# Kernel optimization log

Measured on AMD Instinct MI355X. Metric: run time of the kernel, lower is better.

## Reference

```python
import jax, jax.numpy as jnp
import numpy as np

TAU = 1.0
K_TAU = 1.0
MAX_K = 64


def setup_inputs() -> dict:
    key = jax.random.key(0)
    ks = jax.random.split(key, 6)
    B, S, D, H = 8, 4096, 1024, 2048
    token_embeddings = jax.random.normal(ks[0], (B, S, D), dtype=jnp.float32)
    W1 = jax.random.normal(ks[1], (D, H), dtype=jnp.float32) * (1.0 / np.sqrt(D))
    b1 = jnp.zeros((H,), dtype=jnp.float32)
    W2 = jax.random.normal(ks[2], (H, 1), dtype=jnp.float32) * (1.0 / np.sqrt(H))
    b2 = jnp.zeros((1,), dtype=jnp.float32)
    k_logits = jax.random.normal(ks[3], (MAX_K,), dtype=jnp.float32) * 0.02
    return {"token_embeddings": token_embeddings, "W1": W1, "b1": b1,
            "W2": W2, "b2": b2, "k_logits": k_logits}


def _gumbel(rng, shape):
    u = jax.random.uniform(rng, shape, minval=1e-08, maxval=1.0 - 1e-08)
    return -jnp.log(-jnp.log(u))


def reference(token_embeddings, W1, b1, W2, b2, k_logits):
    B, S, D = token_embeddings.shape
    # scorer: Dense -> relu -> Dense(1), squeeze -> [B, S]
    h = jax.nn.relu(jnp.einsum('bsd,dh->bsh', token_embeddings, W1) + b1)
    importance_logits = (jnp.einsum('bsh,ho->bso', h, W2) + b2)[..., 0]

    rng = jax.random.key(42)  # training rng
    rng1, rng2 = jax.random.split(rng)

    # learnable-k selection (training branch)
    k_gumbel = _gumbel(rng1, k_logits.shape)
    k_soft = jax.nn.softmax((k_logits + k_gumbel) / K_TAU)
    expected_k = jnp.sum(k_soft * jnp.arange(1, MAX_K + 1, dtype=k_soft.dtype))
    k_selected = jnp.argmax(k_soft) + 1  # traced int scalar

    # gumbel-softmax hard top-k over tokens
    perturbed = importance_logits + _gumbel(rng2, importance_logits.shape)
    soft_mask = jax.nn.softmax(perturbed / TAU, axis=-1)  # [B, S]
    # rank of each token (0 = smallest); top-k == rank >= S - k
    rank = jnp.argsort(jnp.argsort(soft_mask, axis=-1), axis=-1)
    hard_mask = (rank >= S - k_selected).astype(soft_mask.dtype)
    selection_mask = jax.lax.stop_gradient(hard_mask - soft_mask) + soft_mask

    filtered_embeddings = token_embeddings * selection_mask[..., None]
    return filtered_embeddings, selection_mask, expected_k
```

## Files before the change

### kernel.cpp

```cpp
#include <hip/hip_runtime.h>
#include <stdint.h>

#define B_BATCH 8
#define S_SEQ   4096
#define D_DIM   1024
#define H_DIM   2048
#define M_TOK   (B_BATCH * S_SEQ)
#define MAXK    64
#define NSPLIT  2

typedef unsigned int u32;
typedef unsigned short u16;
typedef unsigned long long u64;
typedef __attribute__((ext_vector_type(8))) short short8;
typedef __attribute__((ext_vector_type(4))) float f32x4;

#define GLOBAL_AS __attribute__((address_space(1)))
#define LDS_AS    __attribute__((address_space(3)))


#define TF_ROUND(x0, x1, r) { x0 += x1; x1 = ((x1 << r) | (x1 >> (32 - r))); x1 ^= x0; }

__device__ __forceinline__ void tf2x32(u32 k0, u32 k1, u32 x0, u32 x1, u32& o0, u32& o1) {
  u32 k2 = k0 ^ k1 ^ 0x1BD11BDAu;
  x0 += k0; x1 += k1;
  TF_ROUND(x0, x1, 13) TF_ROUND(x0, x1, 15) TF_ROUND(x0, x1, 26) TF_ROUND(x0, x1, 6)
  x0 += k1; x1 += k2 + 1u;
  TF_ROUND(x0, x1, 17) TF_ROUND(x0, x1, 29) TF_ROUND(x0, x1, 16) TF_ROUND(x0, x1, 24)
  x0 += k2; x1 += k0 + 2u;
  TF_ROUND(x0, x1, 13) TF_ROUND(x0, x1, 15) TF_ROUND(x0, x1, 26) TF_ROUND(x0, x1, 6)
  x0 += k0; x1 += k1 + 3u;
  TF_ROUND(x0, x1, 17) TF_ROUND(x0, x1, 29) TF_ROUND(x0, x1, 16) TF_ROUND(x0, x1, 24)
  x0 += k1; x1 += k2 + 4u;
  TF_ROUND(x0, x1, 13) TF_ROUND(x0, x1, 15) TF_ROUND(x0, x1, 26) TF_ROUND(x0, x1, 6)
  x0 += k2; x1 += k0 + 5u;
  o0 = x0; o1 = x1;
}

__device__ __forceinline__ void jax_subkeys(u32& r1a, u32& r1b, u32& r2a, u32& r2b) {
  tf2x32(0u, 42u, 0u, 0u, r1a, r1b);
  tf2x32(0u, 42u, 0u, 1u, r2a, r2b);
}

__device__ __forceinline__ u32 jax_bits32(u32 ka, u32 kb, u32 i) {
  u32 o0, o1;
  tf2x32(ka, kb, 0u, i, o0, o1);
  return o0 ^ o1;
}

__device__ __forceinline__ float jax_uniform_from_bits(u32 bits) {
  float f = __uint_as_float((bits >> 9) | 0x3f800000u) - 1.0f;
  float r = f + 1e-8f;
  return fmaxf(1e-8f, r);
}

__device__ __forceinline__ float gumbel_from_bits(u32 bits) {
  float u = jax_uniform_from_bits(bits);
  return -logf(-logf(u));
}

__device__ __forceinline__ u32 ordf(float v) {
  u32 b = __float_as_uint(v);
  return (b & 0x80000000u) ? ~b : (b | 0x80000000u);
}

__device__ __forceinline__ u64 shflx64(u64 v, int m) {
  unsigned lo = (unsigned)v, hi = (unsigned)(v >> 32);
  lo = (unsigned)__shfl_xor((int)lo, m);
  hi = (unsigned)__shfl_xor((int)hi, m);
  return ((u64)hi << 32) | lo;
}


__device__ __forceinline__ u16 f2bf_rn(float x) {
  u32 u = __float_as_uint(x);
  u32 r = u + 0x7fffu + ((u >> 16) & 1u);
  return (u16)(r >> 16);
}

__device__ __forceinline__ void split1(float x, u16& h, u16& lo) {
  h = f2bf_rn(x);
  float hf = __uint_as_float(((u32)h) << 16);
  lo = f2bf_rn(x - hf);
}


__global__ __launch_bounds__(256) void split_a_kernel(const float* __restrict__ x,
                                                      u16* __restrict__ hi,
                                                      u16* __restrict__ lo) {
  const size_t i = ((size_t)blockIdx.x * 256 + threadIdx.x) * 4;
  float4 v = *(const float4*)(x + i);
  u16 h0, h1, h2, h3, l0, l1, l2, l3;
  split1(v.x, h0, l0); split1(v.y, h1, l1); split1(v.z, h2, l2); split1(v.w, h3, l3);
  u64 hv = (u64)h0 | ((u64)h1 << 16) | ((u64)h2 << 32) | ((u64)h3 << 48);
  u64 lv = (u64)l0 | ((u64)l1 << 16) | ((u64)l2 << 32) | ((u64)l3 << 48);
  *(u64*)(hi + i) = hv;
  *(u64*)(lo + i) = lv;
}

__global__ __launch_bounds__(256) void split_w1t_kernel(const float* __restrict__ W1,
                                                        u16* __restrict__ bhi,
                                                        u16* __restrict__ blo) {
  __shared__ float tile[32][33];
  const int tx = threadIdx.x & 31, ty = threadIdx.x >> 5;
  const int n0 = blockIdx.x * 32, k0 = blockIdx.y * 32;
  #pragma unroll
  for (int r = 0; r < 4; ++r)
    tile[ty + r * 8][tx] = W1[(size_t)(k0 + ty + r * 8) * H_DIM + n0 + tx];
  __syncthreads();
  #pragma unroll
  for (int r = 0; r < 4; ++r) {
    const int n = n0 + ty + r * 8, k = k0 + tx;
    u16 h, l;
    split1(tile[tx][ty + r * 8], h, l);
    bhi[(size_t)n * D_DIM + k] = h;
    blo[(size_t)n * D_DIM + k] = l;
  }
}


__device__ __forceinline__ void stage16(const u16* g, u16* l) {
  __builtin_amdgcn_global_load_lds((const GLOBAL_AS u32*)g, (LDS_AS u32*)l, 16, 0, 0);
}

__global__ __launch_bounds__(256, 2) void scorer_mfma(
    const u16* __restrict__ Ahi, const u16* __restrict__ Alo,
    const u16* __restrict__ Bhi, const u16* __restrict__ Blo,
    const float* __restrict__ b1, const float* __restrict__ W2,
    float* __restrict__ pl) {
  __shared__ u16 smem[8 * 128 * 32];
  u16* sAhi = smem;
  u16* sAlo = smem + 8192;
  u16* sBhi = smem + 16384;
  u16* sBlo = smem + 24576;

  const int tid = threadIdx.x;
  const int w = tid >> 6;
  const int l = tid & 63;

  const int b = blockIdx.x;
  const int xcd = b & 7;
  const int nyb = xcd & 1;
  const int m0 = ((b >> 3) * 4 + (xcd >> 1)) * 128;

  const int rl0 = w * 32 + (l >> 2);
  const int rl1 = rl0 + 16;
  const int kloc0 = (((l & 3) ^ ((rl0 >> 1) & 3)) << 3);
  const int kloc1 = (((l & 3) ^ ((rl1 >> 1) & 3)) << 3);
  const int lb0 = (w * 32) * 32;
  const int lb1 = (w * 32 + 16) * 32;

  int a_off[4], b_off[4];
  #pragma unroll
  for (int i = 0; i < 4; ++i) {
    int row = ((w & 1) << 6) + i * 16 + (l & 15);
    int slot = (l >> 4) ^ ((row >> 1) & 3);
    a_off[i] = row * 32 + slot * 8;
    int nrow = ((w >> 1) << 6) + i * 16 + (l & 15);
    int nslot = (l >> 4) ^ ((nrow >> 1) & 3);
    b_off[i] = nrow * 32 + nslot * 8;
  }

  float logit[4][4];
  #pragma unroll
  for (int i = 0; i < 4; ++i)
    #pragma unroll
    for (int r = 0; r < 4; ++r) logit[i][r] = 0.f;

  for (int t8 = 0; t8 < H_DIM / (128 * NSPLIT); ++t8) {
    const int n0 = nyb * (H_DIM / NSPLIT) + t8 * 128;
    f32x4 acc[4][4];
    #pragma unroll
    for (int i = 0; i < 4; ++i)
      #pragma unroll
      for (int j = 0; j < 4; ++j) acc[i][j] = (f32x4){0.f, 0.f, 0.f, 0.f};

    const u16* pA0h = Ahi + (size_t)(m0 + rl0) * D_DIM + kloc0;
    const u16* pA1h = Ahi + (size_t)(m0 + rl1) * D_DIM + kloc1;
    const u16* pA0l = Alo + (size_t)(m0 + rl0) * D_DIM + kloc0;
    const u16* pA1l = Alo + (size_t)(m0 + rl1) * D_DIM + kloc1;
    const u16* pB0h = Bhi + (size_t)(n0 + rl0) * D_DIM + kloc0;
    const u16* pB1h = Bhi + (size_t)(n0 + rl1) * D_DIM + kloc1;
    const u16* pB0l = Blo + (size_t)(n0 + rl0) * D_DIM + kloc0;
    const u16* pB1l = Blo + (size_t)(n0 + rl1) * D_DIM + kloc1;

    for (int k0 = 0; k0 < D_DIM; k0 += 64) {
      __syncthreads();
      #pragma unroll
      for (int s = 0; s < 2; ++s) {
        const int so = s * 4096;
        const int sk = s * 32;
        stage16(pA0h + sk, sAhi + so + lb0); stage16(pA1h + sk, sAhi + so + lb1);
        stage16(pA0l + sk, sAlo + so + lb0); stage16(pA1l + sk, sAlo + so + lb1);
        stage16(pB0h + sk, sBhi + so + lb0); stage16(pB1h + sk, sBhi + so + lb1);
        stage16(pB0l + sk, sBlo + so + lb0); stage16(pB1l + sk, sBlo + so + lb1);
      }
      pA0h += 64; pA1h += 64; pA0l += 64; pA1l += 64;
      pB0h += 64; pB1h += 64; pB0l += 64; pB1l += 64;
      __syncthreads();

      #pragma unroll
      for (int s = 0; s < 2; ++s) {
        const int so = s * 4096;
        short8 ah[4], al[4], bh[4], bl[4];
        #pragma unroll
        for (int i = 0; i < 4; ++i) {
          ah[i] = *(const short8*)(sAhi + so + a_off[i]);
          al[i] = *(const short8*)(sAlo + so + a_off[i]);
          bh[i] = *(const short8*)(sBhi + so + b_off[i]);
          bl[i] = *(const short8*)(sBlo + so + b_off[i]);
        }
        #pragma unroll
        for (int i = 0; i < 4; ++i)
          #pragma unroll
          for (int j = 0; j < 4; ++j) {
            acc[i][j] = __builtin_amdgcn_mfma_f32_16x16x32_bf16(ah[i], bh[j], acc[i][j], 0, 0, 0);
            acc[i][j] = __builtin_amdgcn_mfma_f32_16x16x32_bf16(ah[i], bl[j], acc[i][j], 0, 0, 0);
            acc[i][j] = __builtin_amdgcn_mfma_f32_16x16x32_bf16(al[i], bh[j], acc[i][j], 0, 0, 0);
          }
      }
    }

    const int nb = n0 + ((w >> 1) << 6);
    #pragma unroll
    for (int j = 0; j < 4; ++j) {
      const int n = nb + j * 16 + (l & 15);
      const float b1v = b1[n];
      const float w2v = W2[n];
      #pragma unroll
      for (int i = 0; i < 4; ++i)
        #pragma unroll
        for (int r = 0; r < 4; ++r)
          logit[i][r] += fmaxf(acc[i][j][r] + b1v, 0.f) * w2v;
    }
  }

  __syncthreads();
  float* red = (float*)smem;
  const int col = (l & 15) + ((w >> 1) << 4);
  #pragma unroll
  for (int i = 0; i < 4; ++i)
    #pragma unroll
    for (int r = 0; r < 4; ++r) {
      const int m = ((w & 1) << 6) + i * 16 + ((l >> 4) << 2) + r;
      red[m * 33 + col] = logit[i][r];
    }
  __syncthreads();
  if (tid < 128) {
    float s = 0.f;
    #pragma unroll
    for (int x = 0; x < 32; ++x) s += red[tid * 33 + x];
    pl[(size_t)nyb * M_TOK + m0 + tid] = s;
  }
}


__global__ __launch_bounds__(256) void scorer_kernel(
    const float* __restrict__ emb, const float* __restrict__ W1,
    const float* __restrict__ b1, const float* __restrict__ W2,
    const float* __restrict__ b2, float* __restrict__ pert) {
  __shared__ float As[16][68];
  __shared__ float Bs[16][132];
  __shared__ float red[64][17];

  const int tid = threadIdx.x;
  const int tx = tid & 15;
  const int ty = tid >> 4;
  const int m0 = blockIdx.x * 64;
  const int at = tid >> 2;
  const int ac = (tid & 3) << 2;
  const int br = tid >> 4;
  const int bc = (tid & 15) << 3;

  float logit[4] = {0.f, 0.f, 0.f, 0.f};

  for (int n0 = 0; n0 < H_DIM; n0 += 128) {
    float acc[4][8];
    #pragma unroll
    for (int i = 0; i < 4; i++)
      #pragma unroll
      for (int j = 0; j < 8; j++) acc[i][j] = 0.f;

    for (int k0 = 0; k0 < D_DIM; k0 += 16) {
      float4 av  = *(const float4*)(emb + (size_t)(m0 + at) * D_DIM + (k0 + ac));
      float4 bv0 = *(const float4*)(W1 + (size_t)(k0 + br) * H_DIM + (n0 + bc));
      float4 bv1 = *(const float4*)(W1 + (size_t)(k0 + br) * H_DIM + (n0 + bc) + 4);
      __syncthreads();
      As[ac + 0][at] = av.x; As[ac + 1][at] = av.y;
      As[ac + 2][at] = av.z; As[ac + 3][at] = av.w;
      *(float4*)&Bs[br][bc]     = bv0;
      *(float4*)&Bs[br][bc + 4] = bv1;
      __syncthreads();
      #pragma unroll
      for (int k = 0; k < 16; k++) {
        float4 a   = *(const float4*)&As[k][ty << 2];
        float4 b0  = *(const float4*)&Bs[k][tx << 3];
        float4 b1v = *(const float4*)&Bs[k][(tx << 3) + 4];
        float aa[4] = {a.x, a.y, a.z, a.w};
        float bb[8] = {b0.x, b0.y, b0.z, b0.w, b1v.x, b1v.y, b1v.z, b1v.w};
        #pragma unroll
        for (int i = 0; i < 4; i++)
          #pragma unroll
          for (int j = 0; j < 8; j++)
            acc[i][j] = fmaf(aa[i], bb[j], acc[i][j]);
      }
    }
    float4 c0 = *(const float4*)(b1 + n0 + (tx << 3));
    float4 c1 = *(const float4*)(b1 + n0 + (tx << 3) + 4);
    float4 w0 = *(const float4*)(W2 + n0 + (tx << 3));
    float4 w1 = *(const float4*)(W2 + n0 + (tx << 3) + 4);
    float cb[8] = {c0.x, c0.y, c0.z, c0.w, c1.x, c1.y, c1.z, c1.w};
    float wb[8] = {w0.x, w0.y, w0.z, w0.w, w1.x, w1.y, w1.z, w1.w};
    #pragma unroll
    for (int i = 0; i < 4; i++)
      #pragma unroll
      for (int j = 0; j < 8; j++) {
        float h = fmaxf(acc[i][j] + cb[j], 0.f);
        logit[i] = fmaf(h, wb[j], logit[i]);
      }
  }

  __syncthreads();
  #pragma unroll
  for (int i = 0; i < 4; i++) red[(ty << 2) + i][tx] = logit[i];
  __syncthreads();

  if (tid < 64) {
    float s = 0.f;
    #pragma unroll
    for (int x = 0; x < 16; x++) s += red[tid][x];
    s += b2[0];
    int t = m0 + tid;
    u32 r1a, r1b, r2a, r2b;
    jax_subkeys(r1a, r1b, r2a, r2b);
    pert[t] = s + gumbel_from_bits(jax_bits32(r2a, r2b, (u32)t));
  }
}


template <bool FROM_PL>
__device__ __forceinline__ void topk_body(const float* kl, const float* pl,
                                          const float* b2, float* mask,
                                          float* expk) {
  const int r = blockIdx.x;
  const int tid = threadIdx.x;
  const int w = tid >> 6, l = tid & 63;
  __shared__ int ksel_sh;
  __shared__ int cnt[2][4];

  u32 r1a, r1b, r2a, r2b;
  jax_subkeys(r1a, r1b, r2a, r2b);

  if (tid < 64) {
    float p = kl[l] + gumbel_from_bits(jax_bits32(r1a, r1b, (u32)l));
    u64 kkey = ((u64)ordf(p) << 32) | (unsigned)(63 - l);
    #pragma unroll
    for (int off = 32; off >= 1; off >>= 1) {
      u64 o = shflx64(kkey, off);
      if (o > kkey) kkey = o;
    }
    if (l == 0) ksel_sh = 64 - (int)(kkey & 0xffffffffu);
    if (r == 0) {
      float m = p;
      #pragma unroll
      for (int off = 32; off >= 1; off >>= 1) m = fmaxf(m, __shfl_xor(m, off));
      float e = expf(p - m);
      float s = e;
      #pragma unroll
      for (int off = 32; off >= 1; off >>= 1) s += __shfl_xor(s, off);
      float v = (e / s) * (float)(l + 1);
      #pragma unroll
      for (int off = 32; off >= 1; off >>= 1) v += __shfl_xor(v, off);
      if (l == 0) expk[0] = v;
    }
  }
  __syncthreads();
  const int k = ksel_sh;
  const float b2v = FROM_PL ? b2[0] : 0.f;

  u64 keys[16];
  #pragma unroll
  for (int j = 0; j < 16; j++) {
    int s = tid + (j << 8);
    int t = (r << 12) + s;
    float v;
    if (FROM_PL) {
      float acc = pl[t];
      #pragma unroll
      for (int q = 1; q < NSPLIT; ++q) acc += pl[(size_t)q * M_TOK + t];
      v = acc + b2v + gumbel_from_bits(jax_bits32(r2a, r2b, (u32)t));
    } else {
      v = mask[t];
    }
    keys[j] = ((u64)ordf(v) << 12) | (unsigned)s;
  }

  u64 lo = 0ull, hi = (1ull << 44) - 1ull;
  int it = 0;
  while (lo < hi) {
    const u64 mid = (lo + hi + 1ull) >> 1;
    int c = 0;
    #pragma unroll
    for (int j = 0; j < 16; j++) c += (keys[j] >= mid) ? 1 : 0;
    #pragma unroll
    for (int off = 32; off >= 1; off >>= 1) c += __shfl_xor(c, off);
    const int buf = it & 1;
    if (l == 0) cnt[buf][w] = c;
    __syncthreads();
    const int tot = cnt[buf][0] + cnt[buf][1] + cnt[buf][2] + cnt[buf][3];
    if (tot >= k) lo = mid; else hi = mid - 1ull;
    ++it;
  }
  const u64 thresh = lo;

  #pragma unroll
  for (int j = 0; j < 16; j++) {
    int s = tid + (j << 8);
    mask[(r << 12) + s] = (keys[j] >= thresh) ? 1.0f : 0.0f;
  }
}

__global__ __launch_bounds__(256) void topk_pl_kernel(const float* __restrict__ kl,
                                                      const float* __restrict__ pl,
                                                      const float* __restrict__ b2,
                                                      float* __restrict__ mask,
                                                      float* __restrict__ expk) {
  topk_body<true>(kl, pl, b2, mask, expk);
}

__global__ __launch_bounds__(256) void topk_kernel(const float* __restrict__ kl,
                                                   float* __restrict__ mask,
                                                   float* __restrict__ expk) {
  topk_body<false>(kl, nullptr, nullptr, mask, expk);
}


__global__ __launch_bounds__(256) void filter_kernel(const float* __restrict__ emb,
                                                     const float* __restrict__ mask,
                                                     float* __restrict__ out) {
  const int t = blockIdx.x;
  const float mk = mask[t];
  const size_t base = (size_t)t * D_DIM + ((size_t)threadIdx.x << 2);
  float4 v = *(const float4*)(emb + base);
  *(float4*)(out + base) = make_float4(v.x * mk, v.y * mk, v.z * mk, v.w * mk);
}


extern "C" void kernel_launch(void* const* d_in, const int* in_sizes, int n_in,
                              void* d_out, int out_size, void* d_ws, size_t ws_size,
                              hipStream_t stream) {
  const float* emb = (const float*)d_in[0];
  const float* W1  = (const float*)d_in[1];
  const float* b1  = (const float*)d_in[2];
  const float* W2  = (const float*)d_in[3];
  const float* b2  = (const float*)d_in[4];
  const float* kl  = (const float*)d_in[5];
  float* out  = (float*)d_out;
  float* mask = out + (size_t)M_TOK * D_DIM;
  float* expk = mask + M_TOK;

  const size_t ws_need = (size_t)H_DIM * D_DIM * 2 * 2 + (size_t)NSPLIT * M_TOK * 4;

  if (ws_size >= ws_need) {
    u16* Ahi = (u16*)d_out;
    u16* Alo = Ahi + (size_t)M_TOK * D_DIM;
    u16* Bhi = (u16*)d_ws;
    u16* Blo = Bhi + (size_t)H_DIM * D_DIM;
    float* pl = (float*)(Blo + (size_t)H_DIM * D_DIM);

    split_a_kernel<<<M_TOK * D_DIM / 1024, 256, 0, stream>>>(emb, Ahi, Alo);
    split_w1t_kernel<<<dim3(H_DIM / 32, D_DIM / 32), 256, 0, stream>>>(W1, Bhi, Blo);
    scorer_mfma<<<M_TOK / 128 * NSPLIT, 256, 0, stream>>>(Ahi, Alo, Bhi, Blo, b1, W2, pl);
    topk_pl_kernel<<<B_BATCH, 256, 0, stream>>>(kl, pl, b2, mask, expk);
  } else {
    scorer_kernel<<<M_TOK / 64, 256, 0, stream>>>(emb, W1, b1, W2, b2, mask);
    topk_kernel<<<B_BATCH, 256, 0, stream>>>(kl, mask, expk);
  }

  filter_kernel<<<M_TOK, 256, 0, stream>>>(emb, mask, out);
}
```

Baseline: 702.8 us.

## Rewrite scorer GEMM as 256x256-tile, 512-thread double-buffered pipelined MFMA kernel

Replaces the 128x128-tile scorer GEMM with a 256-row by 256-column tile per block using 8 waves. A/B fragments are staged into a double-buffered dynamic LDS region through async global-to-LDS loads, interleaved with MFMA phases and gated by explicit vmcnt waits and raw barriers. MFMA issue priority is raised while the MFMAs run. The ReLU/W2 epilogue now reduces across lanes with shuffles into an LDS accumulator. The goal is to hide load latency and increase reuse per LDS byte. The cost is 132 KB of LDS per block, a fixed grid of 256 blocks, and hand-tuned wait counts that are fragile.

```diff
diff --git a/kernel.cpp b/kernel.cpp
--- a/kernel.cpp
+++ b/kernel.cpp
@@ -123,134 +123,173 @@
   __builtin_amdgcn_global_load_lds((const GLOBAL_AS u32*)g, (LDS_AS u32*)l, 16, 0, 0);
 }
 
-__global__ __launch_bounds__(256, 2) void scorer_mfma(
+#define WAITV(N) asm volatile("s_waitcnt vmcnt(" #N ")" ::: "memory")
+#define FENCE()  asm volatile("" ::: "memory")
+
+__global__ __launch_bounds__(512, 2) void scorer_mfma256(
     const u16* __restrict__ Ahi, const u16* __restrict__ Alo,
     const u16* __restrict__ Bhi, const u16* __restrict__ Blo,
     const float* __restrict__ b1, const float* __restrict__ W2,
     float* __restrict__ pl) {
-  __shared__ u16 smem[8 * 128 * 32];
-  u16* sAhi = smem;
-  u16* sAlo = smem + 8192;
-  u16* sBhi = smem + 16384;
-  u16* sBlo = smem + 24576;
+  extern __shared__ u16 smem[];
+  float* red = (float*)(smem + 65536);
 
   const int tid = threadIdx.x;
-  const int w = tid >> 6;
-  const int l = tid & 63;
+  const int w = tid >> 6, l = tid & 63;
+  const int wm = w >> 2, wn = w & 3;
 
   const int b = blockIdx.x;
   const int xcd = b & 7;
   const int nyb = xcd & 1;
-  const int m0 = ((b >> 3) * 4 + (xcd >> 1)) * 128;
-
-  const int rl0 = w * 32 + (l >> 2);
-  const int rl1 = rl0 + 16;
-  const int kloc0 = (((l & 3) ^ ((rl0 >> 1) & 3)) << 3);
-  const int kloc1 = (((l & 3) ^ ((rl1 >> 1) & 3)) << 3);
-  const int lb0 = (w * 32) * 32;
-  const int lb1 = (w * 32 + 16) * 32;
-
-  int a_off[4], b_off[4];
-  #pragma unroll
-  for (int i = 0; i < 4; ++i) {
-    int row = ((w & 1) << 6) + i * 16 + (l & 15);
-    int slot = (l >> 4) ^ ((row >> 1) & 3);
-    a_off[i] = row * 32 + slot * 8;
-    int nrow = ((w >> 1) << 6) + i * 16 + (l & 15);
-    int nslot = (l >> 4) ^ ((nrow >> 1) & 3);
-    b_off[i] = nrow * 32 + nslot * 8;
-  }
-
-  float logit[4][4];
-  #pragma unroll
-  for (int i = 0; i < 4; ++i)
-    #pragma unroll
-    for (int r = 0; r < 4; ++r) logit[i][r] = 0.f;
-
-  for (int t8 = 0; t8 < H_DIM / (128 * NSPLIT); ++t8) {
-    const int n0 = nyb * (H_DIM / NSPLIT) + t8 * 128;
-    f32x4 acc[4][4];
-    #pragma unroll
-    for (int i = 0; i < 4; ++i)
-      #pragma unroll
-      for (int j = 0; j < 4; ++j) acc[i][j] = (f32x4){0.f, 0.f, 0.f, 0.f};
-
-    const u16* pA0h = Ahi + (size_t)(m0 + rl0) * D_DIM + kloc0;
-    const u16* pA1h = Ahi + (size_t)(m0 + rl1) * D_DIM + kloc1;
-    const u16* pA0l = Alo + (size_t)(m0 + rl0) * D_DIM + kloc0;
-    const u16* pA1l = Alo + (size_t)(m0 + rl1) * D_DIM + kloc1;
-    const u16* pB0h = Bhi + (size_t)(n0 + rl0) * D_DIM + kloc0;
-    const u16* pB1h = Bhi + (size_t)(n0 + rl1) * D_DIM + kloc1;
-    const u16* pB0l = Blo + (size_t)(n0 + rl0) * D_DIM + kloc0;
-    const u16* pB1l = Blo + (size_t)(n0 + rl1) * D_DIM + kloc1;
-
-    for (int k0 = 0; k0 < D_DIM; k0 += 64) {
-      __syncthreads();
-      #pragma unroll
-      for (int s = 0; s < 2; ++s) {
-        const int so = s * 4096;
-        const int sk = s * 32;
-        stage16(pA0h + sk, sAhi + so + lb0); stage16(pA1h + sk, sAhi + so + lb1);
-        stage16(pA0l + sk, sAlo + so + lb0); stage16(pA1l + sk, sAlo + so + lb1);
-        stage16(pB0h + sk, sBhi + so + lb0); stage16(pB1h + sk, sBhi + so + lb1);
-        stage16(pB0l + sk, sBlo + so + lb0); stage16(pB1l + sk, sBlo + so + lb1);
-      }
-      pA0h += 64; pA1h += 64; pA0l += 64; pA1l += 64;
-      pB0h += 64; pB1h += 64; pB0l += 64; pB1l += 64;
-      __syncthreads();
-
-      #pragma unroll
-      for (int s = 0; s < 2; ++s) {
-        const int so = s * 4096;
-        short8 ah[4], al[4], bh[4], bl[4];
+  const int m0 = ((b >> 3) * 4 + (xcd >> 1)) * 256;
+
+  const int sig = w * 16 + (l >> 2);
+  const int swz = ((l & 3) ^ ((sig >> 1) & 3)) << 3;
+  const size_t aoffE = (size_t)(m0 + sig + (sig & 64)) * D_DIM + swz;
+  const size_t aoffL = aoffE + (size_t)64 * D_DIM;
+  const size_t boff0 = (size_t)(nyb * 1024 + sig) * D_DIM + swz;
+  const size_t boff1 = boff0 + (size_t)128 * D_DIM;
+  u16* const ldsw = smem + w * 512;
+
+#define ST_AhiE(T) stage16(Ahi + aoffE + (size_t)((((T) & 31) << 5)), ldsw + (((T) & 1) << 15) + 0)
+#define ST_AhiL(T) stage16(Ahi + aoffL + (size_t)((((T) & 31) << 5)), ldsw + (((T) & 1) << 15) + 4096)
+#define ST_AloE(T) stage16(Alo + aoffE + (size_t)((((T) & 31) << 5)), ldsw + (((T) & 1) << 15) + 8192)
+#define ST_AloL(T) stage16(Alo + aoffL + (size_t)((((T) & 31) << 5)), ldsw + (((T) & 1) << 15) + 12288)
+#define ST_BhiH0(T) stage16(Bhi + boff0 + ((size_t)((T) >> 5) << 18) + (size_t)((((T) & 31) << 5)), ldsw + (((T) & 1) << 15) + 16384)
+#define ST_BhiH1(T) stage16(Bhi + boff1 + ((size_t)((T) >> 5) << 18) + (size_t)((((T) & 31) << 5)), ldsw + (((T) & 1) << 15) + 20480)
+#define ST_BloH0(T) stage16(Blo + boff0 + ((size_t)((T) >> 5) << 18) + (size_t)((((T) & 31) << 5)), ldsw + (((T) & 1) << 15) + 24576)
+#define ST_BloH1(T) stage16(Blo + boff1 + ((size_t)((T) >> 5) << 18) + (size_t)((((T) & 31) << 5)), ldsw + (((T) & 1) << 15) + 28672)
+
+  int a_off[8], b_off[4];
+  #pragma unroll
+  for (int mf = 0; mf < 8; ++mf) {
+    int slot = wm * 64 + (mf & 3) * 16 + (l & 15);
+    a_off[mf] = ((mf >> 2) * 4096) + slot * 32 + (((l >> 4) ^ ((slot >> 1) & 3)) << 3);
+  }
+  #pragma unroll
+  for (int nf = 0; nf < 4; ++nf) {
+    int r = wn * 64 + nf * 16 + (l & 15);
+    b_off[nf] = r * 32 + (((l >> 4) ^ ((r >> 1) & 3)) << 3);
+  }
+
+  f32x4 acc[8][4];
+  #pragma unroll
+  for (int mf = 0; mf < 8; ++mf)
+    #pragma unroll
+    for (int nf = 0; nf < 4; ++nf) acc[mf][nf] = (f32x4){0.f, 0.f, 0.f, 0.f};
+
+  const u16* const B0 = smem;
+  const u16* const B1 = smem + 32768;
+  short8 ah0, ah1, al0, al1, bh[4], bl[4];
+
+#define LDA(BASE, MF) \
+  ah0 = *(const short8*)((BASE) + a_off[MF]); \
+  ah1 = *(const short8*)((BASE) + a_off[(MF) + 1]); \
+  al0 = *(const short8*)((BASE) + 8192 + a_off[MF]); \
+  al1 = *(const short8*)((BASE) + 8192 + a_off[(MF) + 1])
+
+#define LDB(BASE) \
+  { _Pragma("unroll") \
+    for (int nf = 0; nf < 4; ++nf) { \
+      bh[nf] = *(const short8*)((BASE) + 16384 + b_off[nf]); \
+      bl[nf] = *(const short8*)((BASE) + 24576 + b_off[nf]); \
+    } }
+
+#define MMA2(MF) \
+  __builtin_amdgcn_s_setprio(1); \
+  { _Pragma("unroll") \
+    for (int nf = 0; nf < 4; ++nf) { \
+      acc[MF][nf] = __builtin_amdgcn_mfma_f32_16x16x32_bf16(ah0, bh[nf], acc[MF][nf], 0, 0, 0); \
+      acc[MF][nf] = __builtin_amdgcn_mfma_f32_16x16x32_bf16(ah0, bl[nf], acc[MF][nf], 0, 0, 0); \
+      acc[MF][nf] = __builtin_amdgcn_mfma_f32_16x16x32_bf16(al0, bh[nf], acc[MF][nf], 0, 0, 0); \
+      acc[(MF) + 1][nf] = __builtin_amdgcn_mfma_f32_16x16x32_bf16(ah1, bh[nf], acc[(MF) + 1][nf], 0, 0, 0); \
+      acc[(MF) + 1][nf] = __builtin_amdgcn_mfma_f32_16x16x32_bf16(ah1, bl[nf], acc[(MF) + 1][nf], 0, 0, 0); \
+      acc[(MF) + 1][nf] = __builtin_amdgcn_mfma_f32_16x16x32_bf16(al1, bh[nf], acc[(MF) + 1][nf], 0, 0, 0); \
+    } } \
+  __builtin_amdgcn_s_setprio(0)
+
+  ST_BhiH0(0); ST_BhiH1(0); ST_BloH0(0); ST_BloH1(0);
+  ST_AhiE(0);  ST_AloE(0);  ST_AhiL(0);  ST_AloL(0);
+  ST_BhiH0(1); ST_BhiH1(1); ST_BloH0(1); ST_BloH1(1);
+  ST_AhiE(1);  ST_AloE(1);
+  WAITV(8);
+  __builtin_amdgcn_s_barrier();
+  FENCE();
+
+  for (int it = 0; it < 64; ++it) {
+    const bool last = (it == 63);
+    const int T1 = 2 * it + 1, T2 = 2 * it + 2, T3 = 2 * it + 3;
+
+    LDB(B0); LDA(B0, 0);
+    ST_AhiL(T1); ST_AloL(T1);
+    MMA2(0);
+    __builtin_amdgcn_s_barrier(); FENCE();
+    LDA(B0, 2);
+    if (!last) { ST_BhiH0(T2); ST_BhiH1(T2); }
+    MMA2(2);
+    if (last) { WAITV(8); } else { WAITV(10); }
+    __builtin_amdgcn_s_barrier(); FENCE();
+    LDA(B0, 4);
+    if (!last) { ST_BloH0(T2); ST_BloH1(T2); }
+    MMA2(4);
+    __builtin_amdgcn_s_barrier(); FENCE();
+    LDA(B0, 6);
+    if (!last) { ST_AhiE(T2); ST_AloE(T2); }
+    MMA2(6);
+    if (last) { WAITV(2); } else { WAITV(8); }
+    __builtin_amdgcn_s_barrier(); FENCE();
+    LDB(B1); LDA(B1, 0);
+    if (!last) { ST_AhiL(T2); ST_AloL(T2); }
+    MMA2(0);
+    __builtin_amdgcn_s_barrier(); FENCE();
+    LDA(B1, 2);
+    if (!last) { ST_BhiH0(T3); ST_BhiH1(T3); }
+    MMA2(2);
+    if (last) { WAITV(0); } else { WAITV(10); }
+    __builtin_amdgcn_s_barrier(); FENCE();
+    LDA(B1, 4);
+    if (!last) { ST_BloH0(T3); ST_BloH1(T3); }
+    MMA2(4);
+    __builtin_amdgcn_s_barrier(); FENCE();
+    LDA(B1, 6);
+    if (!last) { ST_AhiE(T3); ST_AloE(T3); }
+    MMA2(6);
+
+    if ((it & 15) == 15) {
+      const int t8 = it >> 4;
+      const int nb = nyb * 1024 + t8 * 256 + wn * 64 + (l & 15);
+      float b1v[4], w2v[4];
+      #pragma unroll
+      for (int nf = 0; nf < 4; ++nf) { b1v[nf] = b1[nb + nf * 16]; w2v[nf] = W2[nb + nf * 16]; }
+      #pragma unroll
+      for (int mf = 0; mf < 8; ++mf)
         #pragma unroll
-        for (int i = 0; i < 4; ++i) {
-          ah[i] = *(const short8*)(sAhi + so + a_off[i]);
-          al[i] = *(const short8*)(sAlo + so + a_off[i]);
-          bh[i] = *(const short8*)(sBhi + so + b_off[i]);
-          bl[i] = *(const short8*)(sBlo + so + b_off[i]);
+        for (int r = 0; r < 4; ++r) {
+          float p = 0.f;
+          #pragma unroll
+          for (int nf = 0; nf < 4; ++nf)
+            p += fmaxf(acc[mf][nf][r] + b1v[nf], 0.f) * w2v[nf];
+          p += __shfl_xor(p, 1); p += __shfl_xor(p, 2);
+          p += __shfl_xor(p, 4); p += __shfl_xor(p, 8);
+          if ((l & 15) == 0) {
+            float* rp = red + ((wm * 128 + mf * 16 + (l >> 4) * 4 + r) << 2) + wn;
+            if (t8 == 0) *rp = p; else *rp += p;
+          }
         }
+      #pragma unroll
+      for (int mf = 0; mf < 8; ++mf)
         #pragma unroll
-        for (int i = 0; i < 4; ++i)
-          #pragma unroll
-          for (int j = 0; j < 4; ++j) {
-            acc[i][j] = __builtin_amdgcn_mfma_f32_16x16x32_bf16(ah[i], bh[j], acc[i][j], 0, 0, 0);
-            acc[i][j] = __builtin_amdgcn_mfma_f32_16x16x32_bf16(ah[i], bl[j], acc[i][j], 0, 0, 0);
-            acc[i][j] = __builtin_amdgcn_mfma_f32_16x16x32_bf16(al[i], bh[j], acc[i][j], 0, 0, 0);
-          }
-      }
+        for (int nf = 0; nf < 4; ++nf) acc[mf][nf] = (f32x4){0.f, 0.f, 0.f, 0.f};
     }
 
-    const int nb = n0 + ((w >> 1) << 6);
-    #pragma unroll
-    for (int j = 0; j < 4; ++j) {
-      const int n = nb + j * 16 + (l & 15);
-      const float b1v = b1[n];
-      const float w2v = W2[n];
-      #pragma unroll
-      for (int i = 0; i < 4; ++i)
-        #pragma unroll
-        for (int r = 0; r < 4; ++r)
-          logit[i][r] += fmaxf(acc[i][j][r] + b1v, 0.f) * w2v;
-    }
+    WAITV(8);
+    __builtin_amdgcn_s_barrier(); FENCE();
   }
 
   __syncthreads();
-  float* red = (float*)smem;
-  const int col = (l & 15) + ((w >> 1) << 4);
-  #pragma unroll
-  for (int i = 0; i < 4; ++i)
-    #pragma unroll
-    for (int r = 0; r < 4; ++r) {
-      const int m = ((w & 1) << 6) + i * 16 + ((l >> 4) << 2) + r;
-      red[m * 33 + col] = logit[i][r];
-    }
-  __syncthreads();
-  if (tid < 128) {
-    float s = 0.f;
-    #pragma unroll
-    for (int x = 0; x < 32; ++x) s += red[tid * 33 + x];
-    pl[(size_t)nyb * M_TOK + m0 + tid] = s;
+  if (tid < 256) {
+    const float* rp = red + (tid << 2);
+    pl[(size_t)nyb * M_TOK + m0 + tid] = rp[0] + rp[1] + rp[2] + rp[3];
   }
 }
 
@@ -468,9 +507,16 @@
     u16* Blo = Bhi + (size_t)H_DIM * D_DIM;
     float* pl = (float*)(Blo + (size_t)H_DIM * D_DIM);
 
+    static bool attr_done = false;
+    if (!attr_done) {
+      hipFuncSetAttribute(reinterpret_cast<const void*>(scorer_mfma256),
+                          hipFuncAttributeMaxDynamicSharedMemorySize, 135168);
+      attr_done = true;
+    }
+
     split_a_kernel<<<M_TOK * D_DIM / 1024, 256, 0, stream>>>(emb, Ahi, Alo);
     split_w1t_kernel<<<dim3(H_DIM / 32, D_DIM / 32), 256, 0, stream>>>(W1, Bhi, Blo);
-    scorer_mfma<<<M_TOK / 128 * NSPLIT, 256, 0, stream>>>(Ahi, Alo, Bhi, Blo, b1, W2, pl);
+    scorer_mfma256<<<256, 512, 135168, stream>>>(Ahi, Alo, Bhi, Blo, b1, W2, pl);
     topk_pl_kernel<<<B_BATCH, 256, 0, stream>>>(kl, pl, b2, mask, expk);
   } else {
     scorer_kernel<<<M_TOK / 64, 256, 0, stream>>>(emb, W1, b1, W2, b2, mask);
```

Measured after the change: 593.9 us. 15.5% less time.
